# Performance work log

Hardware: AMD Instinct MI355X
Metric: run time of the kernel (lower is better)

The kernel has to match this reference:

```python
import jax, jax.numpy as jnp
import numpy as np

OUT_SIZE = (224, 224)  # (Ho, Wo)


def setup_inputs() -> dict:
    key = jax.random.key(0)
    k1, k2, k3 = jax.random.split(key, 3)
    B, H, W_in, C = 16, 224, 224, 32
    F = 128
    x = jax.random.normal(k1, (B, H, W_in, C), dtype=jnp.float32)
    theta_feat = jax.random.normal(k2, (B, F), dtype=jnp.float32)
    # localisation head params: W small (original inits zeros), b = flattened 2x3 identity
    W = jax.random.normal(k3, (F, 6), dtype=jnp.float32) * 0.01
    b = jnp.array([1.0, 0.0, 0.0, 0.0, 1.0, 0.0], dtype=jnp.float32)
    return {"x": x, "theta_feat": theta_feat, "W": W, "b": b}


def _transform(im, theta, out_size):
    # im: [B,H,W,C], theta: [B,6] -> affine grid sample, border-clamped bilinear
    B, H, W_in, C = im.shape
    Ho, Wo = out_size
    Hf = jnp.float32(H)
    Wf = jnp.float32(W_in)

    # normalized target grid in [-1, 1], homogeneous coords [3, N]
    x_t = jnp.linspace(-1.0, 1.0, Wo, dtype=jnp.float32)
    y_t = jnp.linspace(-1.0, 1.0, Ho, dtype=jnp.float32)
    xg, yg = jnp.meshgrid(x_t, y_t)  # [Ho, Wo]
    grid = jnp.stack([xg.ravel(), yg.ravel(), jnp.ones(Ho * Wo, jnp.float32)])  # [3, N]

    T = theta.reshape(B, 2, 3)
    src = jnp.einsum('bij,jn->bin', T, grid)  # [B, 2, N]
    xs = src[:, 0, :]  # [B, N] in [-1,1]
    ys = src[:, 1, :]

    # map to source pixel coords (original transformer uses width/2, not (width-1)/2)
    xp = (xs + 1.0) * Wf / 2.0
    yp = (ys + 1.0) * Hf / 2.0

    x0 = jnp.floor(xp).astype(jnp.int32)
    x1 = x0 + 1
    y0 = jnp.floor(yp).astype(jnp.int32)
    y1 = y0 + 1
    x0 = jnp.clip(x0, 0, W_in - 1)
    x1 = jnp.clip(x1, 0, W_in - 1)
    y0 = jnp.clip(y0, 0, H - 1)
    y1 = jnp.clip(y1, 0, H - 1)

    x0f = x0.astype(jnp.float32)
    x1f = x1.astype(jnp.float32)
    y0f = y0.astype(jnp.float32)
    y1f = y1.astype(jnp.float32)
    wa = (x1f - xp) * (y1f - yp)
    wb = (x1f - xp) * (yp - y0f)
    wc = (xp - x0f) * (y1f - yp)
    wd = (xp - x0f) * (yp - y0f)

    im_flat = im.reshape(B, H * W_in, C)

    def gather(yy, xx):
        idx = (yy * W_in + xx)[..., None]  # [B, N, 1]
        return jnp.take_along_axis(im_flat, idx, axis=1)  # [B, N, C]

    Ia = gather(y0, x0)
    Ib = gather(y1, x0)
    Ic = gather(y0, x1)
    Id = gather(y1, x1)

    out = (wa[..., None] * Ia + wb[..., None] * Ib
           + wc[..., None] * Ic + wd[..., None] * Id)  # [B, N, C]
    return out.reshape(B, Ho, Wo, C)


def reference(x, theta_feat, W, b):
    theta = jnp.tanh(theta_feat @ W + b)  # [B, 6]
    return _transform(x, theta, OUT_SIZE)
```

## Files before the change

kernel.cpp:

```cpp
#include <hip/hip_runtime.h>
#include <math.h>

#define BATCH 16
#define HIN   224
#define WIN   224
#define CCH   32
#define FDIM  128
#define HOUT  224
#define WOUT  224

#define PIX_PER_BATCH (HOUT * WOUT)
#define BLOCK 256
#define PIX_PER_BLOCK (BLOCK / 8)
#define BLOCKS_PER_BATCH (PIX_PER_BATCH / PIX_PER_BLOCK)
#define NBLOCKS (BATCH * BLOCKS_PER_BATCH)
#define NXCD 8
#define BLOCKS_PER_XCD (NBLOCKS / NXCD)

__global__ void st_theta_kernel(const float* __restrict__ tf,
                                const float* __restrict__ Wm,
                                const float* __restrict__ bv,
                                float* __restrict__ theta) {
    int t = blockIdx.x * blockDim.x + threadIdx.x;
    if (t >= BATCH * 6) return;
    int bi = t / 6;
    int j  = t - bi * 6;
    float acc = bv[j];
    const float* row = tf + bi * FDIM;
#pragma unroll 8
    for (int k = 0; k < FDIM; ++k) {
        acc += row[k] * Wm[k * 6 + j];
    }
    theta[t] = tanhf(acc);
}

__global__ __launch_bounds__(BLOCK) void st_sample_kernel(
        const float* __restrict__ im,
        const float* __restrict__ theta,
        float* __restrict__ out) {

    int bid = blockIdx.x;
    int nb  = (bid & (NXCD - 1)) * BLOCKS_PER_XCD + (bid >> 3);

    int gid = nb * BLOCK + (int)threadIdx.x;

    int p  = gid >> 3;
    int c4 = gid & 7;

    int b   = p / PIX_PER_BATCH;
    int rem = p - b * PIX_PER_BATCH;
    int ho  = rem / WOUT;
    int wo  = rem - ho * WOUT;

    float x_t = -1.0f + (2.0f * (float)wo) / (float)(WOUT - 1);
    float y_t = -1.0f + (2.0f * (float)ho) / (float)(HOUT - 1);

    const float* th = theta + b * 6;
    float t0 = th[0], t1 = th[1], t2 = th[2];
    float t3 = th[3], t4 = th[4], t5 = th[5];

    float xs = t0 * x_t + t1 * y_t + t2;
    float ys = t3 * x_t + t4 * y_t + t5;

    float xp = (xs + 1.0f) * (0.5f * (float)WIN);
    float yp = (ys + 1.0f) * (0.5f * (float)HIN);

    float fx0 = floorf(xp);
    float fy0 = floorf(yp);
    int x0 = (int)fx0;
    int y0 = (int)fy0;
    int x1 = x0 + 1;
    int y1 = y0 + 1;

    x0 = min(max(x0, 0), WIN - 1);
    x1 = min(max(x1, 0), WIN - 1);
    y0 = min(max(y0, 0), HIN - 1);
    y1 = min(max(y1, 0), HIN - 1);

    float x0f = (float)x0, x1f = (float)x1;
    float y0f = (float)y0, y1f = (float)y1;

    float wa = (x1f - xp) * (y1f - yp);
    float wb = (x1f - xp) * (yp - y0f);
    float wc = (xp - x0f) * (y1f - yp);
    float wd = (xp - x0f) * (yp - y0f);

    const float4* imf4 = (const float4*)im;
    size_t base = (size_t)b * (size_t)(HIN * WIN * 8);

    size_t ia = base + ((size_t)(y0 * WIN + x0)) * 8 + c4;
    size_t ib = base + ((size_t)(y1 * WIN + x0)) * 8 + c4;
    size_t ic = base + ((size_t)(y0 * WIN + x1)) * 8 + c4;
    size_t id = base + ((size_t)(y1 * WIN + x1)) * 8 + c4;

    float4 Ia = imf4[ia];
    float4 Ib = imf4[ib];
    float4 Ic = imf4[ic];
    float4 Id = imf4[id];

    float4 o;
    o.x = wa * Ia.x + wb * Ib.x + wc * Ic.x + wd * Id.x;
    o.y = wa * Ia.y + wb * Ib.y + wc * Ic.y + wd * Id.y;
    o.z = wa * Ia.z + wb * Ib.z + wc * Ic.z + wd * Id.z;
    o.w = wa * Ia.w + wb * Ib.w + wc * Ic.w + wd * Id.w;

    ((float4*)out)[gid] = o;
}

extern "C" void kernel_launch(void* const* d_in, const int* in_sizes, int n_in,
                              void* d_out, int out_size, void* d_ws, size_t ws_size,
                              hipStream_t stream) {
    const float* x  = (const float*)d_in[0];
    const float* tf = (const float*)d_in[1];
    const float* Wm = (const float*)d_in[2];
    const float* bv = (const float*)d_in[3];
    float* out = (float*)d_out;

    float* theta = (float*)d_ws;

    st_theta_kernel<<<1, 128, 0, stream>>>(tf, Wm, bv, theta);
    st_sample_kernel<<<NBLOCKS, BLOCK, 0, stream>>>(x, theta, out);
}
```

Baseline: 36.40 us.

## Process two items per thread in sampler and warp-reduce theta matvec

The sampling kernel now handles two float4 output items per thread, computing all addresses first and issuing eight gather loads together so more memory requests are in flight per thread, with half as many blocks. The theta kernel assigns one 64-lane wavefront per output element and reduces with shuffles instead of a serial 128-step loop per thread. Both changes target latency, one in the gather and one in the small serial prologue kernel. The cost is more registers per thread in the sampler and fewer resident blocks to hide latency.

```diff
diff --git a/kernel.cpp b/kernel.cpp
--- a/kernel.cpp
+++ b/kernel.cpp
@@ -11,7 +11,9 @@
 
 #define PIX_PER_BATCH (HOUT * WOUT)
 #define BLOCK 256
-#define PIX_PER_BLOCK (BLOCK / 8)
+#define ITEMS_PER_THREAD 2
+#define ITEMS_PER_BLOCK (BLOCK * ITEMS_PER_THREAD)
+#define PIX_PER_BLOCK (ITEMS_PER_BLOCK / 8)
 #define BLOCKS_PER_BATCH (PIX_PER_BATCH / PIX_PER_BLOCK)
 #define NBLOCKS (BATCH * BLOCKS_PER_BATCH)
 #define NXCD 8
@@ -21,17 +23,21 @@
                                 const float* __restrict__ Wm,
                                 const float* __restrict__ bv,
                                 float* __restrict__ theta) {
-    int t = blockIdx.x * blockDim.x + threadIdx.x;
-    if (t >= BATCH * 6) return;
-    int bi = t / 6;
-    int j  = t - bi * 6;
-    float acc = bv[j];
+    int wid  = (int)((blockIdx.x * blockDim.x + threadIdx.x) >> 6);
+    int lane = (int)(threadIdx.x & 63);
+    if (wid >= BATCH * 6) return;
+    int bi = wid / 6;
+    int j  = wid - bi * 6;
     const float* row = tf + bi * FDIM;
-#pragma unroll 8
-    for (int k = 0; k < FDIM; ++k) {
-        acc += row[k] * Wm[k * 6 + j];
-    }
-    theta[t] = tanhf(acc);
+    float acc = row[lane] * Wm[lane * 6 + j]
+              + row[lane + 64] * Wm[(lane + 64) * 6 + j];
+    acc += __shfl_xor(acc, 32);
+    acc += __shfl_xor(acc, 16);
+    acc += __shfl_xor(acc, 8);
+    acc += __shfl_xor(acc, 4);
+    acc += __shfl_xor(acc, 2);
+    acc += __shfl_xor(acc, 1);
+    if (lane == 0) theta[wid] = tanhf(acc + bv[j]);
 }
 
 __global__ __launch_bounds__(BLOCK) void st_sample_kernel(
@@ -42,69 +48,88 @@
     int bid = blockIdx.x;
     int nb  = (bid & (NXCD - 1)) * BLOCKS_PER_XCD + (bid >> 3);
 
-    int gid = nb * BLOCK + (int)threadIdx.x;
-
-    int p  = gid >> 3;
-    int c4 = gid & 7;
-
-    int b   = p / PIX_PER_BATCH;
-    int rem = p - b * PIX_PER_BATCH;
-    int ho  = rem / WOUT;
-    int wo  = rem - ho * WOUT;
-
-    float x_t = -1.0f + (2.0f * (float)wo) / (float)(WOUT - 1);
-    float y_t = -1.0f + (2.0f * (float)ho) / (float)(HOUT - 1);
+    int b = nb / BLOCKS_PER_BATCH;
 
     const float* th = theta + b * 6;
     float t0 = th[0], t1 = th[1], t2 = th[2];
     float t3 = th[3], t4 = th[4], t5 = th[5];
 
-    float xs = t0 * x_t + t1 * y_t + t2;
-    float ys = t3 * x_t + t4 * y_t + t5;
+    const float4* imf4 = (const float4*)im;
+    float4* of4 = (float4*)out;
+    size_t ibase = (size_t)b * (size_t)(HIN * WIN * 8);
 
-    float xp = (xs + 1.0f) * (0.5f * (float)WIN);
-    float yp = (ys + 1.0f) * (0.5f * (float)HIN);
+    int base = nb * ITEMS_PER_BLOCK + (int)threadIdx.x;
 
-    float fx0 = floorf(xp);
-    float fy0 = floorf(yp);
-    int x0 = (int)fx0;
-    int y0 = (int)fy0;
-    int x1 = x0 + 1;
-    int y1 = y0 + 1;
+    size_t addr[ITEMS_PER_THREAD][4];
+    float  wgt[ITEMS_PER_THREAD][4];
+    int    oidx[ITEMS_PER_THREAD];
 
-    x0 = min(max(x0, 0), WIN - 1);
-    x1 = min(max(x1, 0), WIN - 1);
-    y0 = min(max(y0, 0), HIN - 1);
-    y1 = min(max(y1, 0), HIN - 1);
+#pragma unroll
+    for (int u = 0; u < ITEMS_PER_THREAD; ++u) {
+        int i  = base + u * BLOCK;
+        int p  = i >> 3;
+        int c4 = i & 7;
 
-    float x0f = (float)x0, x1f = (float)x1;
-    float y0f = (float)y0, y1f = (float)y1;
+        int rem = p - b * PIX_PER_BATCH;
+        int ho  = rem / WOUT;
+        int wo  = rem - ho * WOUT;
 
-    float wa = (x1f - xp) * (y1f - yp);
-    float wb = (x1f - xp) * (yp - y0f);
-    float wc = (xp - x0f) * (y1f - yp);
-    float wd = (xp - x0f) * (yp - y0f);
+        float x_t = -1.0f + (2.0f * (float)wo) / (float)(WOUT - 1);
+        float y_t = -1.0f + (2.0f * (float)ho) / (float)(HOUT - 1);
 
-    const float4* imf4 = (const float4*)im;
-    size_t base = (size_t)b * (size_t)(HIN * WIN * 8);
+        float xs = t0 * x_t + t1 * y_t + t2;
+        float ys = t3 * x_t + t4 * y_t + t5;
 
-    size_t ia = base + ((size_t)(y0 * WIN + x0)) * 8 + c4;
-    size_t ib = base + ((size_t)(y1 * WIN + x0)) * 8 + c4;
-    size_t ic = base + ((size_t)(y0 * WIN + x1)) * 8 + c4;
-    size_t id = base + ((size_t)(y1 * WIN + x1)) * 8 + c4;
+        float xp = (xs + 1.0f) * (0.5f * (float)WIN);
+        float yp = (ys + 1.0f) * (0.5f * (float)HIN);
 
-    float4 Ia = imf4[ia];
-    float4 Ib = imf4[ib];
-    float4 Ic = imf4[ic];
-    float4 Id = imf4[id];
+        int x0 = (int)floorf(xp);
+        int y0 = (int)floorf(yp);
+        int x1 = x0 + 1;
+        int y1 = y0 + 1;
 
-    float4 o;
-    o.x = wa * Ia.x + wb * Ib.x + wc * Ic.x + wd * Id.x;
-    o.y = wa * Ia.y + wb * Ib.y + wc * Ic.y + wd * Id.y;
-    o.z = wa * Ia.z + wb * Ib.z + wc * Ic.z + wd * Id.z;
-    o.w = wa * Ia.w + wb * Ib.w + wc * Ic.w + wd * Id.w;
+        x0 = min(max(x0, 0), WIN - 1);
+        x1 = min(max(x1, 0), WIN - 1);
+        y0 = min(max(y0, 0), HIN - 1);
+        y1 = min(max(y1, 0), HIN - 1);
 
-    ((float4*)out)[gid] = o;
+        float x0f = (float)x0, x1f = (float)x1;
+        float y0f = (float)y0, y1f = (float)y1;
+
+        wgt[u][0] = (x1f - xp) * (y1f - yp);
+        wgt[u][1] = (x1f - xp) * (yp - y0f);
+        wgt[u][2] = (xp - x0f) * (y1f - yp);
+        wgt[u][3] = (xp - x0f) * (yp - y0f);
+
+        addr[u][0] = ibase + ((size_t)(y0 * WIN + x0)) * 8 + c4;
+        addr[u][1] = ibase + ((size_t)(y1 * WIN + x0)) * 8 + c4;
+        addr[u][2] = ibase + ((size_t)(y0 * WIN + x1)) * 8 + c4;
+        addr[u][3] = ibase + ((size_t)(y1 * WIN + x1)) * 8 + c4;
+        oidx[u] = i;
+    }
+
+    float4 v[ITEMS_PER_THREAD][4];
+#pragma unroll
+    for (int u = 0; u < ITEMS_PER_THREAD; ++u) {
+#pragma unroll
+        for (int t = 0; t < 4; ++t) {
+            v[u][t] = imf4[addr[u][t]];
+        }
+    }
+
+#pragma unroll
+    for (int u = 0; u < ITEMS_PER_THREAD; ++u) {
+        float4 o;
+        o.x = wgt[u][0] * v[u][0].x + wgt[u][1] * v[u][1].x
+            + wgt[u][2] * v[u][2].x + wgt[u][3] * v[u][3].x;
+        o.y = wgt[u][0] * v[u][0].y + wgt[u][1] * v[u][1].y
+            + wgt[u][2] * v[u][2].y + wgt[u][3] * v[u][3].y;
+        o.z = wgt[u][0] * v[u][0].z + wgt[u][1] * v[u][1].z
+            + wgt[u][2] * v[u][2].z + wgt[u][3] * v[u][3].z;
+        o.w = wgt[u][0] * v[u][0].w + wgt[u][1] * v[u][1].w
+            + wgt[u][2] * v[u][2].w + wgt[u][3] * v[u][3].w;
+        of4[oidx[u]] = o;
+    }
 }
 
 extern "C" void kernel_launch(void* const* d_in, const int* in_sizes, int n_in,
@@ -118,6 +143,6 @@
 
     float* theta = (float*)d_ws;
 
-    st_theta_kernel<<<1, 128, 0, stream>>>(tf, Wm, bv, theta);
+    st_theta_kernel<<<24, 256, 0, stream>>>(tf, Wm, bv, theta);
     st_sample_kernel<<<NBLOCKS, BLOCK, 0, stream>>>(x, theta, out);
 }
```

After: 33.83 us. 1.08x faster.
